# Optimization experiments

Hardware: AMD Instinct MI355X
Metric: run time of the kernel (lower is better)

The kernel has to match this reference:

```python
import jax, jax.numpy as jnp
import numpy as np

N_NODES = 50000
N_EDGES = 800000
IN_CH = 64
HID = 64
HID2 = HID // 2  # 32


def _sage_conv(x, src, dst, w_l, w_r, b, n_nodes):
    """PyG SAGEConv (aggr='mean', root_weight=True):
    out = lin_l(mean_{j in N(i)} x_j) + lin_r(x_i), bias in lin_l.
    Messages flow src -> dst (source_to_target)."""
    msg = x[src]  # [E, d] gather of source features
    summed = jax.ops.segment_sum(msg, dst, num_segments=n_nodes)  # [N, d]
    cnt = jax.ops.segment_sum(jnp.ones((src.shape[0],), x.dtype), dst,
                              num_segments=n_nodes)  # [N]
    mean = summed / jnp.maximum(cnt, 1.0)[:, None]
    return mean @ w_l + b + x @ w_r


def setup_inputs() -> dict:
    key = jax.random.key(0)
    ks = jax.random.split(key, 12)
    s = 0.05
    x = jax.random.normal(ks[0], (N_NODES, IN_CH), dtype=jnp.float32)
    edge_index = jax.random.randint(ks[1], (2, N_EDGES), 0, N_NODES, dtype=jnp.int32)
    return {
        "x": x,
        "edge_index": edge_index,
        # SAGEConv layer 1 (in -> hidden)
        "w1_l": jax.random.normal(ks[2], (IN_CH, HID), dtype=jnp.float32) * s,
        "w1_r": jax.random.normal(ks[3], (IN_CH, HID), dtype=jnp.float32) * s,
        "b1": jnp.zeros((HID,), jnp.float32),
        # SAGEConv layer 2 (hidden -> hidden//2)
        "w2_l": jax.random.normal(ks[4], (HID, HID2), dtype=jnp.float32) * s,
        "w2_r": jax.random.normal(ks[5], (HID, HID2), dtype=jnp.float32) * s,
        "b2": jnp.zeros((HID2,), jnp.float32),
        # classifier MLP: Linear(32,16) -> ReLU -> Linear(16,2)
        "wc1": jax.random.normal(ks[6], (HID2, 16), dtype=jnp.float32) * s,
        "bc1": jnp.zeros((16,), jnp.float32),
        "wc2": jax.random.normal(ks[7], (16, 2), dtype=jnp.float32) * s,
        "bc2": jnp.zeros((2,), jnp.float32),
    }


def reference(x, edge_index, w1_l, w1_r, b1, w2_l, w2_r, b2, wc1, bc1, wc2, bc2):
    src, dst = edge_index[0], edge_index[1]
    n = x.shape[0]
    # Dropout is identity in eval / deterministic reference.
    h = jax.nn.relu(_sage_conv(x, src, dst, w1_l, w1_r, b1, n))
    h = jax.nn.relu(_sage_conv(h, src, dst, w2_l, w2_r, b2, n))
    h = jax.nn.relu(h @ wc1 + bc1)
    out = h @ wc2 + bc2  # [N, 2]
    return out
```

## Files before the change

kernel.cpp:

```cpp
#include <hip/hip_runtime.h>
#include <hip/hip_fp16.h>

#define N_NODES 50000
#define N_EDGES 800000
#define NBINS   391
#define CAP     4096
#define EPB     4096
#define NBLK_E  ((N_EDGES + EPB - 1) / EPB)
#define NTILE   391
#define LSTRIDE 129

__global__ void k_binA(const int* __restrict__ src, const int* __restrict__ dst,
                       int* __restrict__ bincur, int* __restrict__ binned) {
    __shared__ int cnt[NBINS];
    __shared__ int sc[512];
    __shared__ int lpos[NBINS];
    __shared__ int base[NBINS];
    __shared__ int stage[EPB];
    __shared__ unsigned short sbin[EPB];
    int t = threadIdx.x;
    int blkbase = blockIdx.x * EPB;
    int nE = min(EPB, N_EDGES - blkbase);
    for (int i = t; i < NBINS; i += 256) cnt[i] = 0;
    __syncthreads();
    int sv[16], dv[16];
#pragma unroll
    for (int k = 0; k < 16; ++k) {
        int e = blkbase + t + k * 256;
        if (e < N_EDGES) {
            sv[k] = src[e];
            dv[k] = dst[e];
            atomicAdd(&cnt[dv[k] >> 7], 1);
        } else dv[k] = -1;
    }
    __syncthreads();
    sc[t]       = (t < NBINS) ? cnt[t] : 0;
    sc[t + 256] = (t + 256 < NBINS) ? cnt[t + 256] : 0;
    __syncthreads();
    for (int d = 1; d < 512; d <<= 1) {
        int s0 = t, s1 = t + 256;
        int n0 = sc[s0] + ((s0 >= d) ? sc[s0 - d] : 0);
        int n1 = sc[s1] + ((s1 >= d) ? sc[s1 - d] : 0);
        __syncthreads();
        sc[s0] = n0; sc[s1] = n1;
        __syncthreads();
    }
    for (int b = t; b < NBINS; b += 256) {
        int excl = sc[b] - cnt[b];
        lpos[b] = excl;
        sc[b] = excl;
        if (cnt[b] > 0) base[b] = b * CAP + atomicAdd(&bincur[b], cnt[b]);
    }
    __syncthreads();
#pragma unroll
    for (int k = 0; k < 16; ++k) {
        if (dv[k] >= 0) {
            int b = dv[k] >> 7;
            int p = atomicAdd(&lpos[b], 1);
            stage[p] = (sv[k] & 0xFFFF) | ((dv[k] & 127) << 16);
            sbin[p] = (unsigned short)b;
        }
    }
    __syncthreads();
    for (int i = t; i < nE; i += 256) {
        int b = sbin[i];
        int pos = base[b] + (i - sc[b]);
        if (pos < (b + 1) * CAP) binned[pos] = stage[i];
    }
}

__global__ void k_binB(const int* __restrict__ bincur, const int* __restrict__ binned,
                       int* __restrict__ off, unsigned short* __restrict__ deg,
                       int* __restrict__ esrc) {
    __shared__ int cnt[128];
    __shared__ int tmp[128];
    __shared__ int cur[128];
    __shared__ int buf[CAP];
    int b = blockIdx.x, t = threadIdx.x;
    int n0 = b << 7;
    int seg0 = b * CAP;
    int n = min(bincur[b], CAP);
    if (t < 128) cnt[t] = 0;
    __syncthreads();
    for (int i = t; i < n; i += 256) atomicAdd(&cnt[binned[seg0 + i] >> 16], 1);
    __syncthreads();
    int v = (t < 128) ? cnt[t] : 0;
    if (t < 128) tmp[t] = v;
    __syncthreads();
    int val = v;
    for (int d = 1; d < 128; d <<= 1) {
        int add = (t >= d && t < 128) ? tmp[t - d] : 0;
        __syncthreads();
        if (t < 128) { val += add; tmp[t] = val; }
        __syncthreads();
    }
    if (t < 128) {
        int excl = val - v;
        cur[t] = excl;
        int node = n0 + t;
        if (node < N_NODES) {
            off[node] = seg0 + excl;
            deg[node] = (unsigned short)v;
        }
    }
    __syncthreads();
    for (int i = t; i < n; i += 256) {
        int w = binned[seg0 + i];
        int p = atomicAdd(&cur[w >> 16], 1);
        buf[p] = w & 0xFFFF;
    }
    __syncthreads();
    for (int i = t; i < n; i += 256) esrc[seg0 + i] = buf[i];
}

__global__ __launch_bounds__(512) void k_pre1(const float* __restrict__ x,
                                              const float* __restrict__ wl,
                                              const float* __restrict__ wr,
                                              const float* __restrict__ b,
                                              __half* __restrict__ ph,
                                              float* __restrict__ q) {
    __shared__ float sx[64 * LSTRIDE];
    int t = threadIdx.x;
    int g0 = blockIdx.x * 128;
#pragma unroll
    for (int i = 0; i < 4; ++i) {
        int f = t + i * 512;
        int nd = f >> 4, cq = f & 15;
        int gn = g0 + nd;
        float4 v = (gn < N_NODES) ? ((const float4*)x)[(size_t)gn * 16 + cq]
                                  : make_float4(0.f, 0.f, 0.f, 0.f);
        sx[(cq * 4 + 0) * LSTRIDE + nd] = v.x;
        sx[(cq * 4 + 1) * LSTRIDE + nd] = v.y;
        sx[(cq * 4 + 2) * LSTRIDE + nd] = v.z;
        sx[(cq * 4 + 3) * LSTRIDE + nd] = v.w;
    }
    __syncthreads();
    int role = __builtin_amdgcn_readfirstlane(t >> 7);
    int wsel = role >> 1;
    int c0 = (role & 1) * 32;
    int ln = t & 127;
    int node = g0 + ln;
    const float* __restrict__ wm = wsel ? wr : wl;
    float acc[32];
    if (wsel) {
#pragma unroll
        for (int c = 0; c < 32; ++c) acc[c] = b[c0 + c];
    } else {
#pragma unroll
        for (int c = 0; c < 32; ++c) acc[c] = 0.f;
    }
#pragma unroll
    for (int k = 0; k < 64; ++k) {
        float xk = sx[k * LSTRIDE + ln];
#pragma unroll
        for (int c = 0; c < 32; ++c)
            acc[c] = fmaf(xk, wm[k * 64 + c0 + c], acc[c]);
    }
    if (node >= N_NODES) return;
    if (wsel == 0) {
        alignas(16) __half2 hv[16];
#pragma unroll
        for (int i = 0; i < 16; ++i)
            hv[i] = __floats2half2_rn(acc[2 * i], acc[2 * i + 1]);
        float4* op = (float4*)(ph + (size_t)node * 64 + c0);
#pragma unroll
        for (int i = 0; i < 4; ++i) op[i] = ((float4*)hv)[i];
    } else {
        float4* op = (float4*)(q + (size_t)node * 64 + c0);
#pragma unroll
        for (int i = 0; i < 8; ++i)
            op[i] = make_float4(acc[4 * i], acc[4 * i + 1], acc[4 * i + 2], acc[4 * i + 3]);
    }
}

__device__ __forceinline__ void acc8(float* a, float4 rv) {
    const __half2* hp = (const __half2*)&rv;
    float2 f0 = __half22float2(hp[0]), f1 = __half22float2(hp[1]);
    float2 f2 = __half22float2(hp[2]), f3 = __half22float2(hp[3]);
    a[0] += f0.x; a[1] += f0.y; a[2] += f1.x; a[3] += f1.y;
    a[4] += f2.x; a[5] += f2.y; a[6] += f3.x; a[7] += f3.y;
}

__global__ __launch_bounds__(256) void k_agg1(const int* __restrict__ off,
                                              const unsigned short* __restrict__ deg,
                                              const int* __restrict__ esrc,
                                              const __half* __restrict__ ph,
                                              const float* __restrict__ q,
                                              float* __restrict__ h1) {
    int wv = threadIdx.x >> 6, lane = threadIdx.x & 63;
    int h = lane >> 5, l32 = lane & 31;
    int node = blockIdx.x * 8 + wv * 2 + h;
    int eg = l32 >> 3;
    int cg = l32 & 7;
    int s0 = off[node];
    int dv = deg[node];
    int s1 = s0 + dv;
    float a[8] = {0, 0, 0, 0, 0, 0, 0, 0};
    float c2[8] = {0, 0, 0, 0, 0, 0, 0, 0};
    for (int i = s0; i < s1; i += 8) {
        int i0 = i + eg, i1 = i + 4 + eg;
        if (i0 < s1) acc8(a,  *(const float4*)(ph + (size_t)esrc[i0] * 64 + (cg << 3)));
        if (i1 < s1) acc8(c2, *(const float4*)(ph + (size_t)esrc[i1] * 64 + (cg << 3)));
    }
#pragma unroll
    for (int j = 0; j < 8; ++j) a[j] += c2[j];
#pragma unroll
    for (int j = 0; j < 8; ++j) {
        a[j] += __shfl_xor(a[j], 8);
        a[j] += __shfl_xor(a[j], 16);
    }
    if (eg == 0) {
        float inv = 1.0f / fmaxf((float)dv, 1.0f);
        const float4* qp = (const float4*)(q + (size_t)node * 64 + (cg << 3));
        float4 q0 = qp[0], q1 = qp[1];
        float4 o0, o1;
        o0.x = fmaxf(fmaf(a[0], inv, q0.x), 0.f);
        o0.y = fmaxf(fmaf(a[1], inv, q0.y), 0.f);
        o0.z = fmaxf(fmaf(a[2], inv, q0.z), 0.f);
        o0.w = fmaxf(fmaf(a[3], inv, q0.w), 0.f);
        o1.x = fmaxf(fmaf(a[4], inv, q1.x), 0.f);
        o1.y = fmaxf(fmaf(a[5], inv, q1.y), 0.f);
        o1.z = fmaxf(fmaf(a[6], inv, q1.z), 0.f);
        o1.w = fmaxf(fmaf(a[7], inv, q1.w), 0.f);
        float4* op = (float4*)(h1 + (size_t)node * 64 + (cg << 3));
        op[0] = o0; op[1] = o1;
    }
}

__global__ __launch_bounds__(256) void k_pre2(const float* __restrict__ h1,
                                              const float* __restrict__ w2l,
                                              const float* __restrict__ w2r,
                                              const float* __restrict__ b2,
                                              __half* __restrict__ zh,
                                              float* __restrict__ r) {
    __shared__ float sx[64 * LSTRIDE];
    int t = threadIdx.x;
    int g0 = blockIdx.x * 128;
#pragma unroll
    for (int i = 0; i < 8; ++i) {
        int f = t + i * 256;
        int nd = f >> 4, cq = f & 15;
        int gn = g0 + nd;
        float4 v = (gn < N_NODES) ? ((const float4*)h1)[(size_t)gn * 16 + cq]
                                  : make_float4(0.f, 0.f, 0.f, 0.f);
        sx[(cq * 4 + 0) * LSTRIDE + nd] = v.x;
        sx[(cq * 4 + 1) * LSTRIDE + nd] = v.y;
        sx[(cq * 4 + 2) * LSTRIDE + nd] = v.z;
        sx[(cq * 4 + 3) * LSTRIDE + nd] = v.w;
    }
    __syncthreads();
    int role = __builtin_amdgcn_readfirstlane(t >> 7);
    int ln = t & 127;
    int node = g0 + ln;
    const float* __restrict__ wm = role ? w2r : w2l;
    float acc[32];
    if (role) {
#pragma unroll
        for (int c = 0; c < 32; ++c) acc[c] = b2[c];
    } else {
#pragma unroll
        for (int c = 0; c < 32; ++c) acc[c] = 0.f;
    }
#pragma unroll
    for (int k = 0; k < 64; ++k) {
        float xk = sx[k * LSTRIDE + ln];
#pragma unroll
        for (int c = 0; c < 32; ++c)
            acc[c] = fmaf(xk, wm[k * 32 + c], acc[c]);
    }
    if (node >= N_NODES) return;
    if (role == 0) {
        alignas(16) __half2 hv[16];
#pragma unroll
        for (int i = 0; i < 16; ++i)
            hv[i] = __floats2half2_rn(acc[2 * i], acc[2 * i + 1]);
        float4* op = (float4*)(zh + (size_t)node * 32);
#pragma unroll
        for (int i = 0; i < 4; ++i) op[i] = ((float4*)hv)[i];
    } else {
        float4* op = (float4*)(r + (size_t)node * 32);
#pragma unroll
        for (int i = 0; i < 8; ++i)
            op[i] = make_float4(acc[4 * i], acc[4 * i + 1], acc[4 * i + 2], acc[4 * i + 3]);
    }
}

__global__ __launch_bounds__(256) void k_agg2cls(const int* __restrict__ off,
                                                 const unsigned short* __restrict__ deg,
                                                 const int* __restrict__ esrc,
                                                 const __half* __restrict__ zh,
                                                 const float* __restrict__ r,
                                                 const float* __restrict__ wc1,
                                                 const float* __restrict__ bc1,
                                                 const float* __restrict__ wc2,
                                                 const float* __restrict__ bc2,
                                                 float* __restrict__ out) {
    __shared__ float sh2[16 * 33];
    __shared__ float sh3[16 * 17];
    __shared__ float swc1[512];
    __shared__ float sbc1[16];
    __shared__ float swc2[32];
    __shared__ float sbc2[2];
    int t = threadIdx.x;
    swc1[t] = wc1[t];
    swc1[t + 256] = wc1[t + 256];
    if (t < 16) sbc1[t] = bc1[t];
    if (t < 32) swc2[t] = wc2[t];
    if (t < 2)  sbc2[t] = bc2[t];

    int lane = t & 63;
    int l16 = lane & 15;
    int nl = (t >> 4) & 15;
    int node = blockIdx.x * 16 + nl;
    int eg = l16 >> 2;
    int cg = l16 & 3;
    int s0 = off[node];
    int dv = deg[node];
    int s1 = s0 + dv;
    float a[8] = {0, 0, 0, 0, 0, 0, 0, 0};
    float c2[8] = {0, 0, 0, 0, 0, 0, 0, 0};
    for (int i = s0; i < s1; i += 8) {
        int i0 = i + eg, i1 = i + 4 + eg;
        if (i0 < s1) acc8(a,  *(const float4*)(zh + (size_t)esrc[i0] * 32 + (cg << 3)));
        if (i1 < s1) acc8(c2, *(const float4*)(zh + (size_t)esrc[i1] * 32 + (cg << 3)));
    }
#pragma unroll
    for (int j = 0; j < 8; ++j) a[j] += c2[j];
#pragma unroll
    for (int j = 0; j < 8; ++j) {
        a[j] += __shfl_xor(a[j], 4);
        a[j] += __shfl_xor(a[j], 8);
    }
    if (eg == 0) {
        float inv = 1.0f / fmaxf((float)dv, 1.0f);
        const float4* rp = (const float4*)(r + (size_t)node * 32 + (cg << 3));
        float4 r0 = rp[0], r1 = rp[1];
        float* d = sh2 + nl * 33 + (cg << 3);
        d[0] = fmaxf(fmaf(a[0], inv, r0.x), 0.f);
        d[1] = fmaxf(fmaf(a[1], inv, r0.y), 0.f);
        d[2] = fmaxf(fmaf(a[2], inv, r0.z), 0.f);
        d[3] = fmaxf(fmaf(a[3], inv, r0.w), 0.f);
        d[4] = fmaxf(fmaf(a[4], inv, r1.x), 0.f);
        d[5] = fmaxf(fmaf(a[5], inv, r1.y), 0.f);
        d[6] = fmaxf(fmaf(a[6], inv, r1.z), 0.f);
        d[7] = fmaxf(fmaf(a[7], inv, r1.w), 0.f);
    }
    __syncthreads();
    int n = t >> 4, j = t & 15;
    float acc1 = sbc1[j];
#pragma unroll
    for (int k = 0; k < 32; ++k)
        acc1 = fmaf(sh2[n * 33 + k], swc1[k * 16 + j], acc1);
    sh3[n * 17 + j] = fmaxf(acc1, 0.f);
    __syncthreads();
    if (t < 16) {
        int nn = t;
        float o0 = sbc2[0], o1 = sbc2[1];
#pragma unroll
        for (int k = 0; k < 16; ++k) {
            float h3k = sh3[nn * 17 + k];
            o0 = fmaf(h3k, swc2[k * 2 + 0], o0);
            o1 = fmaf(h3k, swc2[k * 2 + 1], o1);
        }
        int gnode = blockIdx.x * 16 + nn;
        *(float2*)(out + (size_t)gnode * 2) = make_float2(o0, o1);
    }
}

extern "C" void kernel_launch(void* const* d_in, const int* in_sizes, int n_in,
                              void* d_out, int out_size, void* d_ws, size_t ws_size,
                              hipStream_t stream) {
    const float* x   = (const float*)d_in[0];
    const int*   ei  = (const int*)d_in[1];
    const int*   src = ei;
    const int*   dst = ei + N_EDGES;
    const float* w1l = (const float*)d_in[2];
    const float* w1r = (const float*)d_in[3];
    const float* b1  = (const float*)d_in[4];
    const float* w2l = (const float*)d_in[5];
    const float* w2r = (const float*)d_in[6];
    const float* b2  = (const float*)d_in[7];
    const float* wc1 = (const float*)d_in[8];
    const float* bc1 = (const float*)d_in[9];
    const float* wc2 = (const float*)d_in[10];
    const float* bc2 = (const float*)d_in[11];
    float* out = (float*)d_out;

    int*   wi     = (int*)d_ws;
    int*   bincur = wi;
    int*   binned = wi + 400;
    int*   esrc   = binned + (size_t)NBINS * CAP;
    int*   off    = esrc + (size_t)NBINS * CAP;
    unsigned short* deg = (unsigned short*)(off + N_NODES);
    float* h1     = (float*)(deg + N_NODES + (N_NODES & 1));
    float* q      = h1 + (size_t)64 * N_NODES;
    float* phf    = q + (size_t)64 * N_NODES;
    __half* ph    = (__half*)phf;
    __half* zh    = (__half*)q;
    float*  r     = q + (size_t)16 * N_NODES;

    hipMemsetAsync(bincur, 0, 400 * sizeof(int), stream);
    k_binA<<<NBLK_E, 256, 0, stream>>>(src, dst, bincur, binned);
    k_binB<<<NBINS, 256, 0, stream>>>(bincur, binned, off, deg, esrc);

    k_pre1<<<NTILE, 512, 0, stream>>>(x, w1l, w1r, b1, ph, q);
    k_agg1<<<N_NODES / 8, 256, 0, stream>>>(off, deg, esrc, ph, q, h1);

    k_pre2<<<NTILE, 256, 0, stream>>>(h1, w2l, w2r, b2, zh, r);
    k_agg2cls<<<N_NODES / 16, 256, 0, stream>>>(off, deg, esrc, zh, r,
                                                wc1, bc1, wc2, bc2, out);
}
```

Before: 195.2 us.

## Merge CSR build and layer-1 projection into one launch; widen gather unroll

The per-bin CSR construction (k_binB) and the layer-1 dense projection (k_pre1) are independent, so they now run as one kernel whose first NBINS blocks do binning and whose remaining blocks do the projection, sharing one shared-memory buffer. This removes a launch and lets the two workloads overlap on the GPU. Separately, both aggregation kernels now unroll the neighbor gather to four independent accumulators, putting more loads in flight per iteration at the cost of more registers. The binning half now runs with 512 threads, and the merged kernel uses the larger shared-memory footprint for every block.

```diff
diff --git a/kernel.cpp b/kernel.cpp
--- a/kernel.cpp
+++ b/kernel.cpp
@@ -69,59 +69,60 @@
     }
 }
 
-__global__ void k_binB(const int* __restrict__ bincur, const int* __restrict__ binned,
-                       int* __restrict__ off, unsigned short* __restrict__ deg,
-                       int* __restrict__ esrc) {
-    __shared__ int cnt[128];
-    __shared__ int tmp[128];
-    __shared__ int cur[128];
-    __shared__ int buf[CAP];
-    int b = blockIdx.x, t = threadIdx.x;
-    int n0 = b << 7;
-    int seg0 = b * CAP;
-    int n = min(bincur[b], CAP);
-    if (t < 128) cnt[t] = 0;
-    __syncthreads();
-    for (int i = t; i < n; i += 256) atomicAdd(&cnt[binned[seg0 + i] >> 16], 1);
-    __syncthreads();
-    int v = (t < 128) ? cnt[t] : 0;
-    if (t < 128) tmp[t] = v;
-    __syncthreads();
-    int val = v;
-    for (int d = 1; d < 128; d <<= 1) {
-        int add = (t >= d && t < 128) ? tmp[t - d] : 0;
-        __syncthreads();
-        if (t < 128) { val += add; tmp[t] = val; }
-        __syncthreads();
-    }
-    if (t < 128) {
-        int excl = val - v;
-        cur[t] = excl;
-        int node = n0 + t;
-        if (node < N_NODES) {
-            off[node] = seg0 + excl;
-            deg[node] = (unsigned short)v;
+__global__ __launch_bounds__(512) void k_binB_pre1(
+        const int* __restrict__ bincur, int* __restrict__ binned,
+        int* __restrict__ off, unsigned short* __restrict__ deg,
+        int* __restrict__ esrc,
+        const float* __restrict__ x,
+        const float* __restrict__ wl, const float* __restrict__ wr,
+        const float* __restrict__ b,
+        __half* __restrict__ ph, float* __restrict__ q) {
+    __shared__ float smem[64 * LSTRIDE];
+    int t = threadIdx.x;
+    int bb = blockIdx.x;
+    if (bb < NBINS) {
+        int* buf = (int*)smem;
+        int* cnt = buf + CAP;
+        int* tmp = cnt + 128;
+        int* cur = tmp + 128;
+        int n0 = bb << 7;
+        int seg0 = bb * CAP;
+        int n = min(bincur[bb], CAP);
+        if (t < 128) cnt[t] = 0;
+        __syncthreads();
+        for (int i = t; i < n; i += 512) atomicAdd(&cnt[binned[seg0 + i] >> 16], 1);
+        __syncthreads();
+        int v = (t < 128) ? cnt[t] : 0;
+        if (t < 128) tmp[t] = v;
+        __syncthreads();
+        int val = v;
+        for (int d = 1; d < 128; d <<= 1) {
+            int add = (t >= d && t < 128) ? tmp[t - d] : 0;
+            __syncthreads();
+            if (t < 128) { val += add; tmp[t] = val; }
+            __syncthreads();
         }
-    }
-    __syncthreads();
-    for (int i = t; i < n; i += 256) {
-        int w = binned[seg0 + i];
-        int p = atomicAdd(&cur[w >> 16], 1);
-        buf[p] = w & 0xFFFF;
-    }
-    __syncthreads();
-    for (int i = t; i < n; i += 256) esrc[seg0 + i] = buf[i];
-}
-
-__global__ __launch_bounds__(512) void k_pre1(const float* __restrict__ x,
-                                              const float* __restrict__ wl,
-                                              const float* __restrict__ wr,
-                                              const float* __restrict__ b,
-                                              __half* __restrict__ ph,
-                                              float* __restrict__ q) {
-    __shared__ float sx[64 * LSTRIDE];
-    int t = threadIdx.x;
-    int g0 = blockIdx.x * 128;
+        if (t < 128) {
+            int excl = val - v;
+            cur[t] = excl;
+            int node = n0 + t;
+            if (node < N_NODES) {
+                off[node] = seg0 + excl;
+                deg[node] = (unsigned short)v;
+            }
+        }
+        __syncthreads();
+        for (int i = t; i < n; i += 512) {
+            int w = binned[seg0 + i];
+            int p = atomicAdd(&cur[w >> 16], 1);
+            buf[p] = w & 0xFFFF;
+        }
+        __syncthreads();
+        for (int i = t; i < n; i += 512) esrc[seg0 + i] = buf[i];
+        return;
+    }
+    float* sx = smem;
+    int g0 = (bb - NBINS) * 128;
 #pragma unroll
     for (int i = 0; i < 4; ++i) {
         int f = t + i * 512;
@@ -195,33 +196,35 @@
     int s0 = off[node];
     int dv = deg[node];
     int s1 = s0 + dv;
-    float a[8] = {0, 0, 0, 0, 0, 0, 0, 0};
-    float c2[8] = {0, 0, 0, 0, 0, 0, 0, 0};
-    for (int i = s0; i < s1; i += 8) {
-        int i0 = i + eg, i1 = i + 4 + eg;
-        if (i0 < s1) acc8(a,  *(const float4*)(ph + (size_t)esrc[i0] * 64 + (cg << 3)));
-        if (i1 < s1) acc8(c2, *(const float4*)(ph + (size_t)esrc[i1] * 64 + (cg << 3)));
-    }
-#pragma unroll
-    for (int j = 0; j < 8; ++j) a[j] += c2[j];
+    float a0[8] = {0,0,0,0,0,0,0,0}, a1[8] = {0,0,0,0,0,0,0,0};
+    float a2[8] = {0,0,0,0,0,0,0,0}, a3[8] = {0,0,0,0,0,0,0,0};
+    for (int i = s0; i < s1; i += 16) {
+        int i0 = i + eg, i1 = i + 4 + eg, i2 = i + 8 + eg, i3 = i + 12 + eg;
+        if (i0 < s1) acc8(a0, *(const float4*)(ph + (size_t)esrc[i0] * 64 + (cg << 3)));
+        if (i1 < s1) acc8(a1, *(const float4*)(ph + (size_t)esrc[i1] * 64 + (cg << 3)));
+        if (i2 < s1) acc8(a2, *(const float4*)(ph + (size_t)esrc[i2] * 64 + (cg << 3)));
+        if (i3 < s1) acc8(a3, *(const float4*)(ph + (size_t)esrc[i3] * 64 + (cg << 3)));
+    }
+#pragma unroll
+    for (int j = 0; j < 8; ++j) a0[j] += a1[j] + (a2[j] + a3[j]);
 #pragma unroll
     for (int j = 0; j < 8; ++j) {
-        a[j] += __shfl_xor(a[j], 8);
-        a[j] += __shfl_xor(a[j], 16);
+        a0[j] += __shfl_xor(a0[j], 8);
+        a0[j] += __shfl_xor(a0[j], 16);
     }
     if (eg == 0) {
         float inv = 1.0f / fmaxf((float)dv, 1.0f);
         const float4* qp = (const float4*)(q + (size_t)node * 64 + (cg << 3));
         float4 q0 = qp[0], q1 = qp[1];
         float4 o0, o1;
-        o0.x = fmaxf(fmaf(a[0], inv, q0.x), 0.f);
-        o0.y = fmaxf(fmaf(a[1], inv, q0.y), 0.f);
-        o0.z = fmaxf(fmaf(a[2], inv, q0.z), 0.f);
-        o0.w = fmaxf(fmaf(a[3], inv, q0.w), 0.f);
-        o1.x = fmaxf(fmaf(a[4], inv, q1.x), 0.f);
-        o1.y = fmaxf(fmaf(a[5], inv, q1.y), 0.f);
-        o1.z = fmaxf(fmaf(a[6], inv, q1.z), 0.f);
-        o1.w = fmaxf(fmaf(a[7], inv, q1.w), 0.f);
+        o0.x = fmaxf(fmaf(a0[0], inv, q0.x), 0.f);
+        o0.y = fmaxf(fmaf(a0[1], inv, q0.y), 0.f);
+        o0.z = fmaxf(fmaf(a0[2], inv, q0.z), 0.f);
+        o0.w = fmaxf(fmaf(a0[3], inv, q0.w), 0.f);
+        o1.x = fmaxf(fmaf(a0[4], inv, q1.x), 0.f);
+        o1.y = fmaxf(fmaf(a0[5], inv, q1.y), 0.f);
+        o1.z = fmaxf(fmaf(a0[6], inv, q1.z), 0.f);
+        o1.w = fmaxf(fmaf(a0[7], inv, q1.w), 0.f);
         float4* op = (float4*)(h1 + (size_t)node * 64 + (cg << 3));
         op[0] = o0; op[1] = o1;
     }
@@ -317,33 +320,35 @@
     int s0 = off[node];
     int dv = deg[node];
     int s1 = s0 + dv;
-    float a[8] = {0, 0, 0, 0, 0, 0, 0, 0};
-    float c2[8] = {0, 0, 0, 0, 0, 0, 0, 0};
-    for (int i = s0; i < s1; i += 8) {
-        int i0 = i + eg, i1 = i + 4 + eg;
-        if (i0 < s1) acc8(a,  *(const float4*)(zh + (size_t)esrc[i0] * 32 + (cg << 3)));
-        if (i1 < s1) acc8(c2, *(const float4*)(zh + (size_t)esrc[i1] * 32 + (cg << 3)));
-    }
-#pragma unroll
-    for (int j = 0; j < 8; ++j) a[j] += c2[j];
+    float a0[8] = {0,0,0,0,0,0,0,0}, a1[8] = {0,0,0,0,0,0,0,0};
+    float a2[8] = {0,0,0,0,0,0,0,0}, a3[8] = {0,0,0,0,0,0,0,0};
+    for (int i = s0; i < s1; i += 16) {
+        int i0 = i + eg, i1 = i + 4 + eg, i2 = i + 8 + eg, i3 = i + 12 + eg;
+        if (i0 < s1) acc8(a0, *(const float4*)(zh + (size_t)esrc[i0] * 32 + (cg << 3)));
+        if (i1 < s1) acc8(a1, *(const float4*)(zh + (size_t)esrc[i1] * 32 + (cg << 3)));
+        if (i2 < s1) acc8(a2, *(const float4*)(zh + (size_t)esrc[i2] * 32 + (cg << 3)));
+        if (i3 < s1) acc8(a3, *(const float4*)(zh + (size_t)esrc[i3] * 32 + (cg << 3)));
+    }
+#pragma unroll
+    for (int j = 0; j < 8; ++j) a0[j] += a1[j] + (a2[j] + a3[j]);
 #pragma unroll
     for (int j = 0; j < 8; ++j) {
-        a[j] += __shfl_xor(a[j], 4);
-        a[j] += __shfl_xor(a[j], 8);
+        a0[j] += __shfl_xor(a0[j], 4);
+        a0[j] += __shfl_xor(a0[j], 8);
     }
     if (eg == 0) {
         float inv = 1.0f / fmaxf((float)dv, 1.0f);
         const float4* rp = (const float4*)(r + (size_t)node * 32 + (cg << 3));
         float4 r0 = rp[0], r1 = rp[1];
         float* d = sh2 + nl * 33 + (cg << 3);
-        d[0] = fmaxf(fmaf(a[0], inv, r0.x), 0.f);
-        d[1] = fmaxf(fmaf(a[1], inv, r0.y), 0.f);
-        d[2] = fmaxf(fmaf(a[2], inv, r0.z), 0.f);
-        d[3] = fmaxf(fmaf(a[3], inv, r0.w), 0.f);
-        d[4] = fmaxf(fmaf(a[4], inv, r1.x), 0.f);
-        d[5] = fmaxf(fmaf(a[5], inv, r1.y), 0.f);
-        d[6] = fmaxf(fmaf(a[6], inv, r1.z), 0.f);
-        d[7] = fmaxf(fmaf(a[7], inv, r1.w), 0.f);
+        d[0] = fmaxf(fmaf(a0[0], inv, r0.x), 0.f);
+        d[1] = fmaxf(fmaf(a0[1], inv, r0.y), 0.f);
+        d[2] = fmaxf(fmaf(a0[2], inv, r0.z), 0.f);
+        d[3] = fmaxf(fmaf(a0[3], inv, r0.w), 0.f);
+        d[4] = fmaxf(fmaf(a0[4], inv, r1.x), 0.f);
+        d[5] = fmaxf(fmaf(a0[5], inv, r1.y), 0.f);
+        d[6] = fmaxf(fmaf(a0[6], inv, r1.z), 0.f);
+        d[7] = fmaxf(fmaf(a0[7], inv, r1.w), 0.f);
     }
     __syncthreads();
     int n = t >> 4, j = t & 15;
@@ -401,9 +406,10 @@
 
     hipMemsetAsync(bincur, 0, 400 * sizeof(int), stream);
     k_binA<<<NBLK_E, 256, 0, stream>>>(src, dst, bincur, binned);
-    k_binB<<<NBINS, 256, 0, stream>>>(bincur, binned, off, deg, esrc);
-
-    k_pre1<<<NTILE, 512, 0, stream>>>(x, w1l, w1r, b1, ph, q);
+
+    k_binB_pre1<<<NBINS + NTILE, 512, 0, stream>>>(bincur, binned, off, deg, esrc,
+                                                   x, w1l, w1r, b1, ph, q);
+
     k_agg1<<<N_NODES / 8, 256, 0, stream>>>(off, deg, esrc, ph, q, h1);
 
     k_pre2<<<NTILE, 256, 0, stream>>>(h1, w2l, w2r, b2, zh, r);
```

Result: faster. 186.5 us (-4.4%).
